# Kernel tuning notes

Hardware: AMD Instinct MI355X
Metric: run time of the kernel (lower is better)

## Reference

```python
import jax, jax.numpy as jnp
import numpy as np

N_NODES = 10000
N_EDGES = 320000
DIM = 256
EDGE_DIM = 64
HEADS = 4
HEAD_DIM = DIM // HEADS
K_HOPS = 3
GAMMA = 0.5
FF_HIDDEN = 512


def setup_inputs() -> dict:
    key = jax.random.key(0)
    ks = jax.random.split(key, 8)
    x = jax.random.normal(ks[0], (N_NODES, DIM), dtype=jnp.float32)
    edge_index = jax.random.randint(ks[1], (2, N_EDGES), 0, N_NODES, dtype=jnp.int64)
    edge_attr = jax.random.normal(ks[2], (N_EDGES, EDGE_DIM), dtype=jnp.float32)
    W_x = jax.random.normal(ks[3], (DIM, DIM), dtype=jnp.float32) / np.sqrt(DIM)
    W_e = jax.random.normal(ks[4], (EDGE_DIM, DIM), dtype=jnp.float32) / np.sqrt(EDGE_DIM)
    att_a = jax.random.normal(ks[5], (HEADS, HEAD_DIM), dtype=jnp.float32) / np.sqrt(HEAD_DIM)
    W_ff1 = jax.random.normal(ks[6], (DIM, FF_HIDDEN), dtype=jnp.float32) / np.sqrt(DIM)
    W_ff2 = jax.random.normal(ks[7], (FF_HIDDEN, DIM), dtype=jnp.float32) / np.sqrt(FF_HIDDEN)
    return {"x": x, "edge_index": edge_index, "edge_attr": edge_attr,
            "W_x": W_x, "W_e": W_e, "att_a": att_a, "W_ff1": W_ff1, "W_ff2": W_ff2}


def reference(x, edge_index, edge_attr, W_x, W_e, att_a, W_ff1, W_ff2):
    N = x.shape[0]
    src, dst = edge_index[0], edge_index[1]

    h0 = x @ W_x                     # (N, H*D) linear node transform
    e = edge_attr @ W_e              # (E, H*D) linear edge transform
    deg = jax.ops.segment_sum(jnp.ones_like(src, dtype=x.dtype), dst,
                              num_segments=N)  # (N,)

    # K-hop propagation with graph elimination: remove gamma-weighted
    # backtracking contribution of the hop-(k-2) state.
    hops = [h0]
    h_prev2 = jnp.zeros_like(h0)
    h_prev1 = h0
    for _ in range(K_HOPS):
        m = jax.nn.relu(h_prev1[src] + e)                       # (E, H*D)
        agg = jax.ops.segment_sum(m, dst, num_segments=N)       # (N, H*D)
        h_k = agg - GAMMA * deg[:, None] * h_prev2
        hops.append(h_k)
        h_prev2, h_prev1 = h_prev1, h_k

    hs = jnp.stack(hops, 0).reshape(K_HOPS + 1, N, HEADS, HEAD_DIM)  # (K+1,N,H,D)

    # Per-head hop attention: query is the hop-0 (center) representation.
    q = hs[0]                                                        # (N,H,D)
    scores = jnp.einsum('hd,knhd->knh', att_a, jnp.tanh(hs + q[None]))
    alpha = jax.nn.softmax(scores, axis=0)                           # (K+1,N,H)
    out = jnp.einsum('knh,knhd->nhd', alpha, hs).reshape(N, DIM)     # concat heads

    # use_ffN: residual feed-forward
    out = out + jax.nn.relu(out @ W_ff1) @ W_ff2

    # wrapper: act (ReLU) + dropout(eval=identity) + residual
    out = jax.nn.relu(out)
    return x + out
```

## Files before the change

### kernel.cpp

```cpp
#include <hip/hip_runtime.h>
#include <hip/hip_bf16.h>

#define N_NODES   10000
#define N_EDGES   320000
#define DIM       256
#define EDGE_DIM  64
#define FF_HIDDEN 512
#define GAMMA     0.5f

typedef __attribute__((ext_vector_type(8))) short bf16x8;
typedef __attribute__((ext_vector_type(4))) float f32x4;

static __device__ __forceinline__ unsigned short f2b(float f)
{
    union { __hip_bfloat16 b; unsigned short u; } c;
    c.b = __float2bfloat16(f);
    return c.u;
}
static __device__ __forceinline__ float b2f(unsigned u)
{
    union { unsigned u32; float f; } c;
    c.u32 = u << 16;
    return c.f;
}

static __device__ __forceinline__ unsigned f2fp8(float f)
{
    union { float f; unsigned u; } c; c.f = f;
    const unsigned s = (c.u >> 24) & 0x80u;
    int v = (int)(((c.u & 0x7FFFFFFFu) + 0x00080000u) >> 20) - 960;
    v = (v < 8) ? 0 : ((v > 126) ? 126 : v);
    return s | (unsigned)v;
}
static __device__ __forceinline__ float fp8tof(unsigned u)
{
    unsigned v = ((u & 0x7Fu) << 4) + 0x3C00u;
    v = (u & 0x78u) ? v : 0u;
    v |= (u & 0x80u) << 8;
    union { unsigned u; float f; } c; c.u = v << 16;
    return c.f;
}

static __device__ __forceinline__ bf16x8 load_a_frag(const float* __restrict__ p)
{
    const float4 f0 = *(const float4*)p;
    const float4 f1 = *(const float4*)(p + 4);
    bf16x8 r;
    r[0] = (short)f2b(f0.x); r[1] = (short)f2b(f0.y);
    r[2] = (short)f2b(f0.z); r[3] = (short)f2b(f0.w);
    r[4] = (short)f2b(f1.x); r[5] = (short)f2b(f1.y);
    r[6] = (short)f2b(f1.z); r[7] = (short)f2b(f1.w);
    return r;
}
static __device__ __forceinline__ float b2fs(unsigned short u)
{
    union { unsigned u32; float f; } c;
    c.u32 = ((unsigned)u) << 16;
    return c.f;
}

__global__ __launch_bounds__(256) void detect_kernel(const unsigned* __restrict__ ei,
                                                     int* __restrict__ flag)
{
    __shared__ int bad;
    if (threadIdx.x == 0) bad = 0;
    __syncthreads();
    int b = 0;
    for (int i = threadIdx.x; i < 1024; i += 256)
        if (ei[2 * i + 1] != 0u) b = 1;
    if (b) atomicAdd(&bad, 1);
    __syncthreads();
    if (threadIdx.x == 0) *flag = (bad == 0) ? 1 : 0;
}

__global__ __launch_bounds__(256) void convert_kernel(const unsigned* __restrict__ ei,
                                                      const int* __restrict__ flag,
                                                      int* __restrict__ src, int* __restrict__ dst,
                                                      int* __restrict__ counts)
{
    const int i = blockIdx.x * 256 + threadIdx.x;
    if (i >= N_EDGES) return;
    const int f = *flag;
    int s, d;
    if (f) { s = (int)ei[2 * i]; d = (int)ei[2 * (N_EDGES + i)]; }
    else   { s = (int)ei[i];     d = (int)ei[N_EDGES + i]; }
    src[i] = s;
    dst[i] = d;
    atomicAdd(&counts[d], 1);
}

__global__ __launch_bounds__(256) void scan_kernel(const int* __restrict__ counts,
                                                   int* __restrict__ row_start)
{
    __shared__ int lds[256];
    const int t = threadIdx.x;
    int vals[40];
    int tot = 0;
    const int base = t * 40;
#pragma unroll
    for (int j = 0; j < 40; ++j) {
        const int idx = base + j;
        const int c = (idx < N_NODES) ? counts[idx] : 0;
        vals[j] = tot;
        tot += c;
    }
    lds[t] = tot;
    __syncthreads();
    for (int off = 1; off < 256; off <<= 1) {
        const int tmp = (t >= off) ? lds[t - off] : 0;
        __syncthreads();
        lds[t] += tmp;
        __syncthreads();
    }
    const int ebase = lds[t] - tot;
#pragma unroll
    for (int j = 0; j < 40; ++j) {
        const int idx = base + j;
        if (idx < N_NODES) row_start[idx] = ebase + vals[j];
    }
    if (t == 0) row_start[N_NODES] = N_EDGES;
}

__global__ __launch_bounds__(256) void fill_kernel(const int* __restrict__ src,
                                                   const int* __restrict__ dst,
                                                   const int* __restrict__ row_start,
                                                   int* __restrict__ fillc,
                                                   int* __restrict__ perm,
                                                   int* __restrict__ csr_src)
{
    const int i = blockIdx.x * 256 + threadIdx.x;
    if (i >= N_EDGES) return;
    const int d = dst[i];
    const int pos = atomicAdd(&fillc[d], 1);
    const int slot = row_start[d] + pos;
    perm[i] = slot;
    csr_src[slot] = src[i];
}

__global__ __launch_bounds__(256) void wconv_kernel(const float* __restrict__ W,
                                                    unsigned short* __restrict__ wT,
                                                    int K, int N)
{
    const int i = blockIdx.x * 256 + threadIdx.x;
    if (i >= K * N) return;
    const int k = i / N, n = i - k * N;
    wT[(size_t)n * K + k] = f2b(W[i]);
}

template <bool ABF16, int MODE>
__global__ __launch_bounds__(256) void wgemm(const void* __restrict__ Av,
                                             const unsigned short* __restrict__ wT,
                                             void* __restrict__ outv,
                                             int M, int K, int N,
                                             const unsigned short* __restrict__ epi_a,
                                             const float* __restrict__ epi_x)
{
    const int tid  = threadIdx.x;
    const int wave = tid >> 6;
    const int lane = tid & 63;
    const int l15  = lane & 15;
    const int l4   = lane >> 4;
    const int m0   = blockIdx.x * 64;
    const int n0   = blockIdx.y * 256 + wave * 64;

    f32x4 acc[4][4];
#pragma unroll
    for (int i = 0; i < 4; ++i)
#pragma unroll
        for (int j = 0; j < 4; ++j) acc[i][j] = f32x4{0.f, 0.f, 0.f, 0.f};

    int rowm[4];
#pragma unroll
    for (int i = 0; i < 4; ++i) rowm[i] = min(m0 + i * 16 + l15, M - 1);

    const int nk = K >> 6;
    for (int kt = 0; kt < nk; ++kt) {
        const int kb = kt * 64 + l4 * 8;
        bf16x8 bfr[2][4], afr[2][4];
#pragma unroll
        for (int ks = 0; ks < 2; ++ks)
#pragma unroll
            for (int j = 0; j < 4; ++j)
                bfr[ks][j] = *(const bf16x8*)(wT + (size_t)(n0 + j * 16 + l15) * K + kb + ks * 32);
#pragma unroll
        for (int ks = 0; ks < 2; ++ks)
#pragma unroll
            for (int i = 0; i < 4; ++i) {
                if (ABF16)
                    afr[ks][i] = *(const bf16x8*)((const unsigned short*)Av + (size_t)rowm[i] * K + kb + ks * 32);
                else
                    afr[ks][i] = load_a_frag((const float*)Av + (size_t)rowm[i] * K + kb + ks * 32);
            }
#pragma unroll
        for (int ks = 0; ks < 2; ++ks)
#pragma unroll
            for (int i = 0; i < 4; ++i)
#pragma unroll
                for (int j = 0; j < 4; ++j)
                    acc[i][j] = __builtin_amdgcn_mfma_f32_16x16x32_bf16(bfr[ks][j], afr[ks][i], acc[i][j], 0, 0, 0);
    }

#pragma unroll
    for (int i = 0; i < 4; ++i) {
        const int m = m0 + i * 16 + l15;
        if (m < M) {
#pragma unroll
            for (int j = 0; j < 4; ++j) {
                const size_t oi = (size_t)m * N + n0 + j * 16 + l4 * 4;
                if (MODE == 2) {
                    const ushort4 ea = *(const ushort4*)(epi_a + oi);
                    const float4  ex = *(const float4*)(epi_x + oi);
                    float4 v;
                    v.x = fmaxf(acc[i][j][0] + b2fs(ea.x), 0.f) + ex.x;
                    v.y = fmaxf(acc[i][j][1] + b2fs(ea.y), 0.f) + ex.y;
                    v.z = fmaxf(acc[i][j][2] + b2fs(ea.z), 0.f) + ex.z;
                    v.w = fmaxf(acc[i][j][3] + b2fs(ea.w), 0.f) + ex.w;
                    *(float4*)((float*)outv + oi) = v;
                } else {
                    float a0 = acc[i][j][0], a1 = acc[i][j][1];
                    float a2 = acc[i][j][2], a3 = acc[i][j][3];
                    if (MODE == 1) {
                        a0 = fmaxf(a0, 0.f); a1 = fmaxf(a1, 0.f);
                        a2 = fmaxf(a2, 0.f); a3 = fmaxf(a3, 0.f);
                    }
                    ushort4 u;
                    u.x = f2b(a0); u.y = f2b(a1); u.z = f2b(a2); u.w = f2b(a3);
                    *(ushort4*)((unsigned short*)outv + oi) = u;
                }
            }
        }
    }
}

__global__ __launch_bounds__(256) void egemm_fp8(const float* __restrict__ A,
                                                 const unsigned short* __restrict__ wT,
                                                 unsigned char* __restrict__ e_out,
                                                 const int* __restrict__ perm)
{
    __shared__ unsigned char et[64 * 272];
    const int tid  = threadIdx.x;
    const int wave = tid >> 6;
    const int lane = tid & 63;
    const int l15  = lane & 15;
    const int l4   = lane >> 4;
    const int wc0  = wave * 64;
    const int m0   = blockIdx.x * 64;

    bf16x8 bfr[2][4];
#pragma unroll
    for (int ks = 0; ks < 2; ++ks)
#pragma unroll
        for (int j = 0; j < 4; ++j)
            bfr[ks][j] = *(const bf16x8*)(wT + (size_t)(wc0 + j * 16 + l15) * 64 + ks * 32 + l4 * 8);

    bf16x8 afr[2][4];
#pragma unroll
    for (int ks = 0; ks < 2; ++ks)
#pragma unroll
        for (int i = 0; i < 4; ++i)
            afr[ks][i] = load_a_frag(A + (size_t)(m0 + i * 16 + l15) * 64 + ks * 32 + l4 * 8);

    f32x4 acc[4][4];
#pragma unroll
    for (int i = 0; i < 4; ++i)
#pragma unroll
        for (int j = 0; j < 4; ++j) acc[i][j] = f32x4{0.f, 0.f, 0.f, 0.f};
#pragma unroll
    for (int ks = 0; ks < 2; ++ks)
#pragma unroll
        for (int i = 0; i < 4; ++i)
#pragma unroll
            for (int j = 0; j < 4; ++j)
                acc[i][j] = __builtin_amdgcn_mfma_f32_16x16x32_bf16(bfr[ks][j], afr[ks][i], acc[i][j], 0, 0, 0);

#pragma unroll
    for (int i = 0; i < 4; ++i)
#pragma unroll
        for (int j = 0; j < 4; ++j) {
            const unsigned p = f2fp8(acc[i][j][0])
                             | (f2fp8(acc[i][j][1]) << 8)
                             | (f2fp8(acc[i][j][2]) << 16)
                             | (f2fp8(acc[i][j][3]) << 24);
            *(unsigned*)(&et[(i * 16 + l15) * 272 + wc0 + j * 16 + l4 * 4]) = p;
        }
    __syncthreads();

    const int row  = tid >> 2;
    const int orow = perm[m0 + row];
    const unsigned char* sp = et + row * 272 + (tid & 3) * 64;
    unsigned char* dp = e_out + (size_t)orow * 256 + (tid & 3) * 64;
#pragma unroll
    for (int v = 0; v < 4; ++v)
        *(uint4*)(dp + v * 16) = *(const uint4*)(sp + v * 16);
}

__global__ __launch_bounds__(256) void hop_kernel(const unsigned short* __restrict__ h_prev1,
                                                  const unsigned short* __restrict__ h_prev2,
                                                  const unsigned char* __restrict__ e,
                                                  const int* __restrict__ row_start,
                                                  const int* __restrict__ csr_src,
                                                  unsigned short* __restrict__ h_out)
{
    const int wave = threadIdx.x >> 6;
    const int lane = threadIdx.x & 63;
    const int n  = blockIdx.x * 4 + wave;
    const int dd = blockIdx.y * 128 + lane * 2;
    const int rb = row_start[n];
    const int re = row_start[n + 1];

    float ax = 0.f, ay = 0.f;
    int s = rb;
    for (; s + 8 <= re; s += 8) {
        int idx[8];
        unsigned short ev[8];
        unsigned hv[8];
#pragma unroll
        for (int u = 0; u < 8; ++u) idx[u] = csr_src[s + u];
#pragma unroll
        for (int u = 0; u < 8; ++u)
            ev[u] = *(const unsigned short*)(e + (size_t)(s + u) * 256 + dd);
#pragma unroll
        for (int u = 0; u < 8; ++u)
            hv[u] = *(const unsigned*)(h_prev1 + (size_t)idx[u] * DIM + dd);
#pragma unroll
        for (int u = 0; u < 8; ++u) {
            ax += fmaxf(b2f(hv[u] & 0xFFFFu) + fp8tof(ev[u] & 255u), 0.f);
            ay += fmaxf(b2f(hv[u] >> 16)     + fp8tof((unsigned)(ev[u] >> 8)), 0.f);
        }
    }
    for (; s < re; ++s) {
        const int sr = csr_src[s];
        const unsigned short ev = *(const unsigned short*)(e + (size_t)s * 256 + dd);
        const unsigned hv = *(const unsigned*)(h_prev1 + (size_t)sr * DIM + dd);
        ax += fmaxf(b2f(hv & 0xFFFFu) + fp8tof(ev & 255u), 0.f);
        ay += fmaxf(b2f(hv >> 16)     + fp8tof((unsigned)(ev >> 8)), 0.f);
    }
    if (h_prev2) {
        const float gd = GAMMA * (float)(re - rb);
        const unsigned p2 = *(const unsigned*)(h_prev2 + (size_t)n * DIM + dd);
        ax -= gd * b2f(p2 & 0xFFFFu);
        ay -= gd * b2f(p2 >> 16);
    }
    *(unsigned*)(h_out + (size_t)n * DIM + dd) =
        ((unsigned)f2b(ay) << 16) | (unsigned)f2b(ax);
}

__global__ __launch_bounds__(256) void attn_kernel(const unsigned short* __restrict__ h0,
                                                   const unsigned short* __restrict__ h1,
                                                   const unsigned short* __restrict__ h2,
                                                   const unsigned short* __restrict__ h3,
                                                   const float* __restrict__ att_a,
                                                   unsigned short* __restrict__ out)
{
    const int n = blockIdx.x;
    const int t = threadIdx.x;
    const size_t i = (size_t)n * DIM + t;
    const float q = b2fs(h0[i]);
    float hk[4];
    hk[0] = q; hk[1] = b2fs(h1[i]); hk[2] = b2fs(h2[i]); hk[3] = b2fs(h3[i]);
    const float a = att_a[t];
    float sc[4];
#pragma unroll
    for (int k = 0; k < 4; ++k) {
        float v = tanhf(hk[k] + q) * a;
#pragma unroll
        for (int off = 32; off > 0; off >>= 1)
            v += __shfl_xor(v, off, 64);
        sc[k] = v;
    }
    const float mx = fmaxf(fmaxf(sc[0], sc[1]), fmaxf(sc[2], sc[3]));
    float ex[4], se = 0.f;
#pragma unroll
    for (int k = 0; k < 4; ++k) { ex[k] = __expf(sc[k] - mx); se += ex[k]; }
    const float inv = 1.f / se;
    float o = 0.f;
#pragma unroll
    for (int k = 0; k < 4; ++k) o += ex[k] * inv * hk[k];
    out[i] = f2b(o);
}

extern "C" void kernel_launch(void* const* d_in, const int* in_sizes, int n_in,
                              void* d_out, int out_size, void* d_ws, size_t ws_size,
                              hipStream_t stream)
{
    const float*    x         = (const float*)d_in[0];
    const unsigned* ei        = (const unsigned*)d_in[1];
    const float*    edge_attr = (const float*)d_in[2];
    const float*    W_x       = (const float*)d_in[3];
    const float*    W_e       = (const float*)d_in[4];
    const float*    att_a     = (const float*)d_in[5];
    const float*    W_ff1     = (const float*)d_in[6];
    const float*    W_ff2     = (const float*)d_in[7];

    char* ws = (char*)d_ws;
    size_t off = 0;
    auto alloc = [&](size_t bytes) -> void* {
        void* p = ws + off;
        off = (off + bytes + 255) & ~(size_t)255;
        return p;
    };
    int*   flag      = (int*)alloc(4);
    int*   src32     = (int*)alloc((size_t)N_EDGES * 4);
    int*   dst32     = (int*)alloc((size_t)N_EDGES * 4);
    int*   counts    = (int*)alloc((size_t)2 * N_NODES * 4);
    int*   fillc     = counts + N_NODES;
    int*   row_start = (int*)alloc((size_t)(N_NODES + 1) * 4);
    int*   perm      = (int*)alloc((size_t)N_EDGES * 4);
    int*   csr_src   = (int*)alloc((size_t)N_EDGES * 4);
    unsigned char*  e_fp8 = (unsigned char*)alloc((size_t)N_EDGES * DIM);
    unsigned short* h0b   = (unsigned short*)alloc((size_t)N_NODES * DIM * 2);
    unsigned short* h1b   = (unsigned short*)alloc((size_t)N_NODES * DIM * 2);
    unsigned short* h2b   = (unsigned short*)alloc((size_t)N_NODES * DIM * 2);
    unsigned short* h3b   = (unsigned short*)alloc((size_t)N_NODES * DIM * 2);
    unsigned short* attnb = (unsigned short*)alloc((size_t)N_NODES * DIM * 2);
    unsigned short* hidb  = (unsigned short*)alloc((size_t)N_NODES * FF_HIDDEN * 2);
    unsigned short* wxT   = (unsigned short*)alloc((size_t)DIM * DIM * 2);
    unsigned short* weT   = (unsigned short*)alloc((size_t)DIM * EDGE_DIM * 2);
    unsigned short* wff1T = (unsigned short*)alloc((size_t)FF_HIDDEN * DIM * 2);
    unsigned short* wff2T = (unsigned short*)alloc((size_t)DIM * FF_HIDDEN * 2);
    if (off > ws_size) return;

    const int egrid = (N_EDGES + 255) / 256;

    hipMemsetAsync(counts, 0, (size_t)2 * N_NODES * 4, stream);
    detect_kernel<<<1, 256, 0, stream>>>(ei, flag);
    convert_kernel<<<egrid, 256, 0, stream>>>(ei, flag, src32, dst32, counts);
    scan_kernel<<<1, 256, 0, stream>>>(counts, row_start);
    fill_kernel<<<egrid, 256, 0, stream>>>(src32, dst32, row_start, fillc, perm, csr_src);

    wconv_kernel<<<(DIM * DIM + 255) / 256, 256, 0, stream>>>(W_x, wxT, DIM, DIM);
    wconv_kernel<<<(EDGE_DIM * DIM + 255) / 256, 256, 0, stream>>>(W_e, weT, EDGE_DIM, DIM);
    wconv_kernel<<<(DIM * FF_HIDDEN + 255) / 256, 256, 0, stream>>>(W_ff1, wff1T, DIM, FF_HIDDEN);
    wconv_kernel<<<(FF_HIDDEN * DIM + 255) / 256, 256, 0, stream>>>(W_ff2, wff2T, FF_HIDDEN, DIM);

    wgemm<false, 0><<<dim3(157, 1), 256, 0, stream>>>(x, wxT, h0b,
        N_NODES, DIM, DIM, nullptr, nullptr);
    egemm_fp8<<<N_EDGES / 64, 256, 0, stream>>>(edge_attr, weT, e_fp8, perm);

    hop_kernel<<<dim3(N_NODES / 4, 2), 256, 0, stream>>>(h0b, nullptr, e_fp8, row_start, csr_src, h1b);
    hop_kernel<<<dim3(N_NODES / 4, 2), 256, 0, stream>>>(h1b, h0b,     e_fp8, row_start, csr_src, h2b);
    hop_kernel<<<dim3(N_NODES / 4, 2), 256, 0, stream>>>(h2b, h1b,     e_fp8, row_start, csr_src, h3b);

    attn_kernel<<<N_NODES, 256, 0, stream>>>(h0b, h1b, h2b, h3b, att_a, attnb);

    wgemm<true, 1><<<dim3(157, 2), 256, 0, stream>>>(attnb, wff1T, hidb,
        N_NODES, DIM, FF_HIDDEN, nullptr, nullptr);
    wgemm<true, 2><<<dim3(157, 1), 256, 0, stream>>>(hidb, wff2T, d_out,
        N_NODES, FF_HIDDEN, DIM, attnb, x);
}
```

Before: 348.6 us.

## Fuse edge-transform GEMM into hop kernels, recomputing edge features per hop

Result: slower. 439.5 us (+26.1%).

```diff
diff --git a/kernel.cpp b/kernel.cpp
--- a/kernel.cpp
+++ b/kernel.cpp
@@ -7,6 +7,8 @@
 #define EDGE_DIM  64
 #define FF_HIDDEN 512
 #define GAMMA     0.5f
+#define CHUNK     192
+#define VSTR      264
 
 typedef __attribute__((ext_vector_type(8))) short bf16x8;
 typedef __attribute__((ext_vector_type(4))) float f32x4;
@@ -17,10 +19,10 @@
     c.b = __float2bfloat16(f);
     return c.u;
 }
-static __device__ __forceinline__ float b2f(unsigned u)
+static __device__ __forceinline__ float b2fs(unsigned short u)
 {
     union { unsigned u32; float f; } c;
-    c.u32 = u << 16;
+    c.u32 = ((unsigned)u) << 16;
     return c.f;
 }
 
@@ -51,12 +53,6 @@
     r[4] = (short)f2b(f1.x); r[5] = (short)f2b(f1.y);
     r[6] = (short)f2b(f1.z); r[7] = (short)f2b(f1.w);
     return r;
-}
-static __device__ __forceinline__ float b2fs(unsigned short u)
-{
-    union { unsigned u32; float f; } c;
-    c.u32 = ((unsigned)u) << 16;
-    return c.f;
 }
 
 __global__ __launch_bounds__(256) void detect_kernel(const unsigned* __restrict__ ei,
@@ -125,7 +121,7 @@
                                                    const int* __restrict__ dst,
                                                    const int* __restrict__ row_start,
                                                    int* __restrict__ fillc,
-                                                   int* __restrict__ perm,
+                                                   int* __restrict__ csr_eid,
                                                    int* __restrict__ csr_src)
 {
     const int i = blockIdx.x * 256 + threadIdx.x;
@@ -133,7 +129,7 @@
     const int d = dst[i];
     const int pos = atomicAdd(&fillc[d], 1);
     const int slot = row_start[d] + pos;
-    perm[i] = slot;
+    csr_eid[slot] = i;
     csr_src[slot] = src[i];
 }
 
@@ -145,6 +141,19 @@
     if (i >= K * N) return;
     const int k = i / N, n = i - k * N;
     wT[(size_t)n * K + k] = f2b(W[i]);
+}
+
+__global__ __launch_bounds__(256) void ea_conv(const float* __restrict__ ea,
+                                               const int* __restrict__ csr_eid,
+                                               unsigned short* __restrict__ out)
+{
+    const int slot = blockIdx.x * 16 + (threadIdx.x >> 4);
+    const int l = threadIdx.x & 15;
+    const int eid = csr_eid[slot];
+    const float4 f = *(const float4*)(ea + (size_t)eid * EDGE_DIM + l * 4);
+    ushort4 u;
+    u.x = f2b(f.x); u.y = f2b(f.y); u.z = f2b(f.z); u.w = f2b(f.w);
+    *(ushort4*)(out + (size_t)slot * EDGE_DIM + l * 4) = u;
 }
 
 template <bool ABF16, int MODE>
@@ -232,117 +241,111 @@
     }
 }
 
-__global__ __launch_bounds__(256) void egemm_fp8(const float* __restrict__ A,
-                                                 const unsigned short* __restrict__ wT,
-                                                 unsigned char* __restrict__ e_out,
-                                                 const int* __restrict__ perm)
-{
-    __shared__ unsigned char et[64 * 272];
+__global__ __launch_bounds__(256) void fused_hop(const unsigned short* __restrict__ h_prev1,
+                                                 const unsigned short* __restrict__ h_prev2,
+                                                 const unsigned short* __restrict__ ea,
+                                                 const unsigned short* __restrict__ weT,
+                                                 const int* __restrict__ row_start,
+                                                 const int* __restrict__ csr_src,
+                                                 unsigned short* __restrict__ h_out)
+{
+    __shared__ __align__(16) unsigned char val[CHUNK * VSTR];
+
     const int tid  = threadIdx.x;
     const int wave = tid >> 6;
     const int lane = tid & 63;
     const int l15  = lane & 15;
     const int l4   = lane >> 4;
     const int wc0  = wave * 64;
-    const int m0   = blockIdx.x * 64;
+
+    const int n0    = blockIdx.x * 4;
+    const int rbase = row_start[n0];
+    const int rend  = row_start[n0 + 4];
+    const int n     = n0 + wave;
+    const int rb    = row_start[n];
+    const int re    = row_start[n + 1];
 
     bf16x8 bfr[2][4];
 #pragma unroll
     for (int ks = 0; ks < 2; ++ks)
 #pragma unroll
         for (int j = 0; j < 4; ++j)
-            bfr[ks][j] = *(const bf16x8*)(wT + (size_t)(wc0 + j * 16 + l15) * 64 + ks * 32 + l4 * 8);
-
-    bf16x8 afr[2][4];
-#pragma unroll
-    for (int ks = 0; ks < 2; ++ks)
-#pragma unroll
-        for (int i = 0; i < 4; ++i)
-            afr[ks][i] = load_a_frag(A + (size_t)(m0 + i * 16 + l15) * 64 + ks * 32 + l4 * 8);
-
-    f32x4 acc[4][4];
-#pragma unroll
-    for (int i = 0; i < 4; ++i)
-#pragma unroll
-        for (int j = 0; j < 4; ++j) acc[i][j] = f32x4{0.f, 0.f, 0.f, 0.f};
-#pragma unroll
-    for (int ks = 0; ks < 2; ++ks)
-#pragma unroll
-        for (int i = 0; i < 4; ++i)
-#pragma unroll
-            for (int j = 0; j < 4; ++j)
-                acc[i][j] = __builtin_amdgcn_mfma_f32_16x16x32_bf16(bfr[ks][j], afr[ks][i], acc[i][j], 0, 0, 0);
-
-#pragma unroll
-    for (int i = 0; i < 4; ++i)
-#pragma unroll
-        for (int j = 0; j < 4; ++j) {
-            const unsigned p = f2fp8(acc[i][j][0])
-                             | (f2fp8(acc[i][j][1]) << 8)
-                             | (f2fp8(acc[i][j][2]) << 16)
-                             | (f2fp8(acc[i][j][3]) << 24);
-            *(unsigned*)(&et[(i * 16 + l15) * 272 + wc0 + j * 16 + l4 * 4]) = p;
+            bfr[ks][j] = *(const bf16x8*)(weT + (size_t)(wc0 + j * 16 + l15) * 64 + ks * 32 + l4 * 8);
+
+    float hx = 0.f, hy = 0.f, hz = 0.f, hw = 0.f;
+
+    for (int c0 = rbase; c0 < rend; c0 += CHUNK) {
+        const int cn = min(CHUNK, rend - c0);
+        __syncthreads();
+
+        for (int rt = 0; rt * 16 < cn; ++rt) {
+            const int arow = min(c0 + rt * 16 + l15, N_EDGES - 1);
+            bf16x8 afr[2];
+#pragma unroll
+            for (int ks = 0; ks < 2; ++ks)
+                afr[ks] = *(const bf16x8*)(ea + (size_t)arow * 64 + ks * 32 + l4 * 8);
+            f32x4 acc[4];
+#pragma unroll
+            for (int j = 0; j < 4; ++j) acc[j] = f32x4{0.f, 0.f, 0.f, 0.f};
+#pragma unroll
+            for (int ks = 0; ks < 2; ++ks)
+#pragma unroll
+                for (int j = 0; j < 4; ++j)
+                    acc[j] = __builtin_amdgcn_mfma_f32_16x16x32_bf16(bfr[ks][j], afr[ks], acc[j], 0, 0, 0);
+#pragma unroll
+            for (int j = 0; j < 4; ++j) {
+                const unsigned p = f2fp8(acc[j][0])
+                                 | (f2fp8(acc[j][1]) << 8)
+                                 | (f2fp8(acc[j][2]) << 16)
+                                 | (f2fp8(acc[j][3]) << 24);
+                *(unsigned*)(&val[(rt * 16 + l15) * VSTR + wc0 + j * 16 + l4 * 4]) = p;
+            }
         }
-    __syncthreads();
-
-    const int row  = tid >> 2;
-    const int orow = perm[m0 + row];
-    const unsigned char* sp = et + row * 272 + (tid & 3) * 64;
-    unsigned char* dp = e_out + (size_t)orow * 256 + (tid & 3) * 64;
-#pragma unroll
-    for (int v = 0; v < 4; ++v)
-        *(uint4*)(dp + v * 16) = *(const uint4*)(sp + v * 16);
-}
-
-__global__ __launch_bounds__(256) void hop_kernel(const unsigned short* __restrict__ h_prev1,
-                                                  const unsigned short* __restrict__ h_prev2,
-                                                  const unsigned char* __restrict__ e,
-                                                  const int* __restrict__ row_start,
-                                                  const int* __restrict__ csr_src,
-                                                  unsigned short* __restrict__ h_out)
-{
-    const int wave = threadIdx.x >> 6;
-    const int lane = threadIdx.x & 63;
-    const int n  = blockIdx.x * 4 + wave;
-    const int dd = blockIdx.y * 128 + lane * 2;
-    const int rb = row_start[n];
-    const int re = row_start[n + 1];
-
-    float ax = 0.f, ay = 0.f;
-    int s = rb;
-    for (; s + 8 <= re; s += 8) {
-        int idx[8];
-        unsigned short ev[8];
-        unsigned hv[8];
-#pragma unroll
-        for (int u = 0; u < 8; ++u) idx[u] = csr_src[s + u];
-#pragma unroll
-        for (int u = 0; u < 8; ++u)
-            ev[u] = *(const unsigned short*)(e + (size_t)(s + u) * 256 + dd);
-#pragma unroll
-        for (int u = 0; u < 8; ++u)
-            hv[u] = *(const unsigned*)(h_prev1 + (size_t)idx[u] * DIM + dd);
-#pragma unroll
-        for (int u = 0; u < 8; ++u) {
-            ax += fmaxf(b2f(hv[u] & 0xFFFFu) + fp8tof(ev[u] & 255u), 0.f);
-            ay += fmaxf(b2f(hv[u] >> 16)     + fp8tof((unsigned)(ev[u] >> 8)), 0.f);
+        __syncthreads();
+
+        const int sb = max(rb, c0);
+        const int se = min(re, c0 + cn);
+        int s = sb;
+        for (; s + 8 <= se; s += 8) {
+            int sr[8];
+            unsigned ev[8];
+            ushort4 hv[8];
+#pragma unroll
+            for (int u = 0; u < 8; ++u) sr[u] = csr_src[s + u];
+#pragma unroll
+            for (int u = 0; u < 8; ++u)
+                ev[u] = *(const unsigned*)(&val[(s + u - c0) * VSTR + lane * 4]);
+#pragma unroll
+            for (int u = 0; u < 8; ++u)
+                hv[u] = *(const ushort4*)(h_prev1 + (size_t)sr[u] * DIM + lane * 4);
+#pragma unroll
+            for (int u = 0; u < 8; ++u) {
+                hx += fmaxf(b2fs(hv[u].x) + fp8tof(ev[u] & 255u), 0.f);
+                hy += fmaxf(b2fs(hv[u].y) + fp8tof((ev[u] >> 8) & 255u), 0.f);
+                hz += fmaxf(b2fs(hv[u].z) + fp8tof((ev[u] >> 16) & 255u), 0.f);
+                hw += fmaxf(b2fs(hv[u].w) + fp8tof(ev[u] >> 24), 0.f);
+            }
         }
-    }
-    for (; s < re; ++s) {
-        const int sr = csr_src[s];
-        const unsigned short ev = *(const unsigned short*)(e + (size_t)s * 256 + dd);
-        const unsigned hv = *(const unsigned*)(h_prev1 + (size_t)sr * DIM + dd);
-        ax += fmaxf(b2f(hv & 0xFFFFu) + fp8tof(ev & 255u), 0.f);
-        ay += fmaxf(b2f(hv >> 16)     + fp8tof((unsigned)(ev >> 8)), 0.f);
-    }
+        for (; s < se; ++s) {
+            const int sr = csr_src[s];
+            const unsigned ev = *(const unsigned*)(&val[(s - c0) * VSTR + lane * 4]);
+            const ushort4 hv = *(const ushort4*)(h_prev1 + (size_t)sr * DIM + lane * 4);
+            hx += fmaxf(b2fs(hv.x) + fp8tof(ev & 255u), 0.f);
+            hy += fmaxf(b2fs(hv.y) + fp8tof((ev >> 8) & 255u), 0.f);
+            hz += fmaxf(b2fs(hv.z) + fp8tof((ev >> 16) & 255u), 0.f);
+            hw += fmaxf(b2fs(hv.w) + fp8tof(ev >> 24), 0.f);
+        }
+    }
+
     if (h_prev2) {
         const float gd = GAMMA * (float)(re - rb);
-        const unsigned p2 = *(const unsigned*)(h_prev2 + (size_t)n * DIM + dd);
-        ax -= gd * b2f(p2 & 0xFFFFu);
-        ay -= gd * b2f(p2 >> 16);
-    }
-    *(unsigned*)(h_out + (size_t)n * DIM + dd) =
-        ((unsigned)f2b(ay) << 16) | (unsigned)f2b(ax);
+        const ushort4 p2 = *(const ushort4*)(h_prev2 + (size_t)n * DIM + lane * 4);
+        hx -= gd * b2fs(p2.x); hy -= gd * b2fs(p2.y);
+        hz -= gd * b2fs(p2.z); hw -= gd * b2fs(p2.w);
+    }
+    ushort4 o;
+    o.x = f2b(hx); o.y = f2b(hy); o.z = f2b(hz); o.w = f2b(hw);
+    *(ushort4*)(h_out + (size_t)n * DIM + lane * 4) = o;
 }
 
 __global__ __launch_bounds__(256) void attn_kernel(const unsigned short* __restrict__ h0,
@@ -405,9 +408,9 @@
     int*   counts    = (int*)alloc((size_t)2 * N_NODES * 4);
     int*   fillc     = counts + N_NODES;
     int*   row_start = (int*)alloc((size_t)(N_NODES + 1) * 4);
-    int*   perm      = (int*)alloc((size_t)N_EDGES * 4);
+    int*   csr_eid   = (int*)alloc((size_t)N_EDGES * 4);
     int*   csr_src   = (int*)alloc((size_t)N_EDGES * 4);
-    unsigned char*  e_fp8 = (unsigned char*)alloc((size_t)N_EDGES * DIM);
+    unsigned short* ea_bf = (unsigned short*)alloc((size_t)N_EDGES * EDGE_DIM * 2);
     unsigned short* h0b   = (unsigned short*)alloc((size_t)N_NODES * DIM * 2);
     unsigned short* h1b   = (unsigned short*)alloc((size_t)N_NODES * DIM * 2);
     unsigned short* h2b   = (unsigned short*)alloc((size_t)N_NODES * DIM * 2);
@@ -426,20 +429,21 @@
     detect_kernel<<<1, 256, 0, stream>>>(ei, flag);
     convert_kernel<<<egrid, 256, 0, stream>>>(ei, flag, src32, dst32, counts);
     scan_kernel<<<1, 256, 0, stream>>>(counts, row_start);
-    fill_kernel<<<egrid, 256, 0, stream>>>(src32, dst32, row_start, fillc, perm, csr_src);
+    fill_kernel<<<egrid, 256, 0, stream>>>(src32, dst32, row_start, fillc, csr_eid, csr_src);
 
     wconv_kernel<<<(DIM * DIM + 255) / 256, 256, 0, stream>>>(W_x, wxT, DIM, DIM);
     wconv_kernel<<<(EDGE_DIM * DIM + 255) / 256, 256, 0, stream>>>(W_e, weT, EDGE_DIM, DIM);
     wconv_kernel<<<(DIM * FF_HIDDEN + 255) / 256, 256, 0, stream>>>(W_ff1, wff1T, DIM, FF_HIDDEN);
     wconv_kernel<<<(FF_HIDDEN * DIM + 255) / 256, 256, 0, stream>>>(W_ff2, wff2T, FF_HIDDEN, DIM);
 
+    ea_conv<<<N_EDGES / 16, 256, 0, stream>>>(edge_attr, csr_eid, ea_bf);
+
     wgemm<false, 0><<<dim3(157, 1), 256, 0, stream>>>(x, wxT, h0b,
         N_NODES, DIM, DIM, nullptr, nullptr);
-    egemm_fp8<<<N_EDGES / 64, 256, 0, stream>>>(edge_attr, weT, e_fp8, perm);
-
-    hop_kernel<<<dim3(N_NODES / 4, 2), 256, 0, stream>>>(h0b, nullptr, e_fp8, row_start, csr_src, h1b);
-    hop_kernel<<<dim3(N_NODES / 4, 2), 256, 0, stream>>>(h1b, h0b,     e_fp8, row_start, csr_src, h2b);
-    hop_kernel<<<dim3(N_NODES / 4, 2), 256, 0, stream>>>(h2b, h1b,     e_fp8, row_start, csr_src, h3b);
+
+    fused_hop<<<N_NODES / 4, 256, 0, stream>>>(h0b, nullptr, ea_bf, weT, row_start, csr_src, h1b);
+    fused_hop<<<N_NODES / 4, 256, 0, stream>>>(h1b, h0b,     ea_bf, weT, row_start, csr_src, h2b);
+    fused_hop<<<N_NODES / 4, 256, 0, stream>>>(h2b, h1b,     ea_bf, weT, row_start, csr_src, h3b);
 
     attn_kernel<<<N_NODES, 256, 0, stream>>>(h0b, h1b, h2b, h3b, att_a, attnb);
 
```
